# Performance work log

Measured on AMD Instinct MI355X. Metric: run time of the kernel, lower is better.

## Reference

```python
import jax, jax.numpy as jnp
import numpy as np

G, NPG, H, F, L = 2000, 16, 128, 28, 6   # graphs, nodes/graph, hidden, feat_dim, num_convs
N = G * NPG                               # 32000 nodes


def _build_graph():
    rng = np.random.default_rng(0)
    # global edges: all ordered intra-molecule pairs (dense radius graph)
    ii, jj = np.nonzero(1 - np.eye(NPG, dtype=np.int64))          # 240 pairs
    goff = np.arange(G, dtype=np.int64)[:, None] * NPG
    sg = (goff + ii[None]).ravel()
    dg = (goff + jj[None]).ravel()
    # local bond edges: ring per molecule, both directions
    li = np.arange(NPG, dtype=np.int64); lj = (li + 1) % NPG
    li2 = np.concatenate([li, lj]); lj2 = np.concatenate([lj, li])  # 32 per graph
    sl = (goff + li2[None]).ravel()
    dl = (goff + lj2[None]).ravel()
    etr = rng.integers(1, 22, size=(G, 2 * NPG)).astype(np.int64)   # bond types r
    etp = rng.integers(1, 22, size=(G, 2 * NPG)).astype(np.int64)   # bond types p
    # global types: local bond type where a bond exists, else 0 (clamped -1 sentinel)
    gidx = np.arange(G)[:, None]
    Tr = np.zeros((G, NPG, NPG), np.int64); Tp = np.zeros_like(Tr)
    Tr[gidx, li2[None], lj2[None]] = etr
    Tp[gidx, li2[None], lj2[None]] = etp
    egr = Tr[gidx, ii[None], jj[None]].ravel()
    egp = Tp[gidx, ii[None], jj[None]].ravel()
    return (np.stack([sl, dl]), etr.ravel(), etp.ravel(),
            np.stack([sg, dg]), egr, egp)


def setup_inputs() -> dict:
    key = jax.random.key(0)
    ks = jax.random.split(key, 24)
    eil, etr, etp, eig, egr, egp = _build_graph()
    n = lambda k, shp, fan: jax.random.normal(k, shp, jnp.float32) / np.sqrt(fan)
    inp = {
        'atom_type': jax.random.randint(ks[0], (N,), 0, 100),
        'r_feat': jax.random.normal(ks[1], (N, F), jnp.float32),
        'p_feat': jax.random.normal(ks[2], (N, F), jnp.float32),
        'pos': jax.random.normal(ks[3], (N, 3), jnp.float32),
        'edge_index_local': jnp.asarray(eil),
        'edge_type_r': jnp.asarray(etr),
        'edge_type_p': jnp.asarray(etp),
        'edge_index_global': jnp.asarray(eig),
        'edge_type_global_r': jnp.asarray(egr),
        'edge_type_global_p': jnp.asarray(egp),
        'bond_emb': n(ks[4], (100, H), 1.0),
        'atom_emb': n(ks[5], (100, H // 2), 1.0),
        'atom_feat_W': n(ks[6], (F, H // 2), F),
        'Wl': n(ks[7], (L, 4 * H, H), 4 * H), 'bl': jnp.zeros((L, H), jnp.float32),
        'Wg': n(ks[8], (L, 2 * H + 1, H), 2 * H + 1), 'bg': jnp.zeros((L, H), jnp.float32),
        'Wn': n(ks[9], (L, 2 * H, H), 2 * H), 'bn': jnp.zeros((L, H), jnp.float32),
        'W0': n(ks[10], (2 * H, H), 2 * H), 'b0': jnp.zeros((H,), jnp.float32),
        'W1': n(ks[11], (H, H // 2), H), 'b1': jnp.zeros((H // 2,), jnp.float32),
        'W2': n(ks[12], (H // 2, 1), H // 2), 'b2': jnp.zeros((1,), jnp.float32),
    }
    return inp


def reference(atom_type, r_feat, p_feat, pos,
              edge_index_local, edge_type_r, edge_type_p,
              edge_index_global, edge_type_global_r, edge_type_global_p,
              bond_emb, atom_emb, atom_feat_W,
              Wl, bl, Wg, bg, Wn, bn, W0, b0, W1, b1, W2, b2):
    num_nodes = atom_type.shape[0]
    # embedding gathers
    e_r = bond_emb[edge_type_r]            # [El,H]
    e_p = bond_emb[edge_type_p]
    e_gr = bond_emb[edge_type_global_r]    # [Eg,H]
    e_gp = bond_emb[edge_type_global_p]
    fr = r_feat @ atom_feat_W              # [N,H/2]
    fp = p_feat @ atom_feat_W
    h = jnp.concatenate([atom_emb[atom_type] + fr, fp - fr], axis=-1)  # [N,H]
    sl, dl = edge_index_local[0], edge_index_local[1]
    sg, dg = edge_index_global[0], edge_index_global[1]
    d2 = jnp.sum((pos[sg] - pos[dg]) ** 2, axis=-1, keepdims=True)     # [Eg,1]
    # EGNN mixed-2D encoder: local (bond) + global (radius) message passing
    for l in range(Wl.shape[0]):
        m_loc = jax.nn.silu(jnp.concatenate([h[sl], h[dl], e_r, e_p], -1) @ Wl[l] + bl[l])
        m_glb = jax.nn.silu(jnp.concatenate([h[sg], h[dg], d2], -1) @ Wg[l] + bg[l])
        agg = (jax.ops.segment_sum(m_loc, dl, num_segments=num_nodes)
               + jax.ops.segment_sum(m_glb, dg, num_segments=num_nodes))
        h = h + jax.nn.silu(jnp.concatenate([h, agg], -1) @ Wn[l] + bn[l])
    # node/edge pair products + output MLP (grad_dist_mlp), sigma_edge = 1.0
    h_pair = jnp.concatenate([h[sg] * h[dg], e_gr * e_gp], axis=-1)    # [Eg,2H]
    x = jax.nn.relu(h_pair @ W0 + b0)
    x = jax.nn.relu(x @ W1 + b1)
    edge_inv = x @ W2 + b2                                             # [Eg,1]
    return edge_inv
```

## Files before the change

### kernel.cpp

```cpp
#include <hip/hip_runtime.h>


#define G_GRAPHS 2000
#define NPG 16
#define HID 128
#define FDIM 28
#define NLAYER 6
#define NNODES 32000
#define EL_PER_G 32
#define EG_PER_G 240
#define EL_TOT (G_GRAPHS*EL_PER_G)
#define EG_TOT (G_GRAPHS*EG_PER_G)
#define TMAX 32

#define MC(r_, c_) ((r_)*HID + ((c_) ^ (((r_) & 7) << 3)))

typedef __attribute__((ext_vector_type(8))) short bf16x8;
typedef __attribute__((ext_vector_type(4))) float f32x4;

__device__ __forceinline__ float silu_f(float x) {
    return x * __builtin_amdgcn_rcpf(1.0f + __expf(-x));
}
__device__ __forceinline__ int clampT(int t) {
    return t < 0 ? 0 : (t > TMAX-1 ? TMAX-1 : t);
}
__device__ __forceinline__ unsigned short bf16_rne(float x) {
    unsigned u = __float_as_uint(x);
    return (unsigned short)((u + 0x7FFFu + ((u >> 16) & 1u)) >> 16);
}
__device__ __forceinline__ void split2(float x, unsigned short &hi, unsigned short &lo) {
    hi = bf16_rne(x);
    float fh = __uint_as_float((unsigned)hi << 16);
    lo = bf16_rne(x - fh);
}

__device__ __forceinline__ unsigned cvtpk(float a, float b) {
    unsigned r;
    asm("v_cvt_pk_bf16_f32 %0, %1, %2" : "=v"(r) : "v"(a), "v"(b));
    return r;
}

__device__ __forceinline__ void split8(const float* vv, bf16x8& h8, bf16x8& l8) {
    union { unsigned u[4]; bf16x8 v; } H, L;
    #pragma unroll
    for (int i = 0; i < 4; i++) {
        unsigned hp = cvtpk(vv[2*i], vv[2*i+1]);
        float fh0 = __uint_as_float(hp << 16);
        float fh1 = __uint_as_float(hp & 0xffff0000u);
        H.u[i] = hp;
        L.u[i] = cvtpk(vv[2*i] - fh0, vv[2*i+1] - fh1);
    }
    h8 = H.v; l8 = L.v;
}

template<int NT>
__device__ __forceinline__ void mm_nt_f32(const float* __restrict__ abuf,
                                          const unsigned short* __restrict__ Bh,
                                          const unsigned short* __restrict__ Bl,
                                          int ctbase, int lane, f32x4* acc) {
    const int n = lane & 15, kq = lane >> 4;
    const int sw = (n & 7) << 3;
    const float* ap = abuf + n*HID;
    const unsigned short* bh = Bh + ((size_t)(ctbase*4)*64 + lane)*8;
    const unsigned short* bl = Bl + ((size_t)(ctbase*4)*64 + lane)*8;
    #pragma unroll 1
    for (int kt = 0; kt < 4; kt++) {
        int idx = (kt*32 + kq*8) ^ sw;
        float4 v0 = *(const float4*)(ap + idx);
        float4 v1 = *(const float4*)(ap + idx + 4);
        float vv[8] = {v0.x, v0.y, v0.z, v0.w, v1.x, v1.y, v1.z, v1.w};
        bf16x8 ah, al;
        split8(vv, ah, al);
        const unsigned short* ph = bh;
        const unsigned short* pl = bl;
        #pragma unroll
        for (int t = 0; t < NT; t++) {
            bf16x8 vh = *(const bf16x8*)ph;
            bf16x8 vl = *(const bf16x8*)pl;
            acc[t] = __builtin_amdgcn_mfma_f32_16x16x32_bf16(ah, vh, acc[t], 0, 0, 0);
            acc[t] = __builtin_amdgcn_mfma_f32_16x16x32_bf16(ah, vl, acc[t], 0, 0, 0);
            acc[t] = __builtin_amdgcn_mfma_f32_16x16x32_bf16(al, vh, acc[t], 0, 0, 0);
            ph += 2048;
            pl += 2048;
        }
        bh += 512;
        bl += 512;
    }
}

__device__ __forceinline__ f32x4 mm_ct_s16(const short* __restrict__ ahbuf,
                                           const short* __restrict__ albuf,
                                           const unsigned short* __restrict__ Bh,
                                           const unsigned short* __restrict__ Bl,
                                           int ct, int lane, f32x4 acc) {
    const int n = lane & 15, kq = lane >> 4;
    const unsigned short* bh = Bh + ((size_t)(ct*4)*64 + lane)*8;
    const unsigned short* bl = Bl + ((size_t)(ct*4)*64 + lane)*8;
    #pragma unroll 1
    for (int kt = 0; kt < 4; kt++) {
        int sidx = (n*HID + kt*32 + kq*8) ^ ((n & 7) << 3);
        bf16x8 ah = *(const bf16x8*)(ahbuf + sidx);
        bf16x8 al = *(const bf16x8*)(albuf + sidx);
        bf16x8 vh = *(const bf16x8*)bh;
        bf16x8 vl = *(const bf16x8*)bl;
        acc = __builtin_amdgcn_mfma_f32_16x16x32_bf16(ah, vh, acc, 0, 0, 0);
        acc = __builtin_amdgcn_mfma_f32_16x16x32_bf16(ah, vl, acc, 0, 0, 0);
        acc = __builtin_amdgcn_mfma_f32_16x16x32_bf16(al, vh, acc, 0, 0, 0);
        bh += 512;
        bl += 512;
    }
    return acc;
}

__global__ void __launch_bounds__(256) k_pack(
    const float* __restrict__ Wg, const float* __restrict__ Wl,
    const float* __restrict__ Wn, const float* __restrict__ W0,
    const float* __restrict__ W1,
    unsigned short* __restrict__ encPh, unsigned short* __restrict__ encPl,
    unsigned short* __restrict__ w0Ph, unsigned short* __restrict__ w0Pl,
    unsigned short* __restrict__ w1Ph, unsigned short* __restrict__ w1Pl)
{
    int b = blockIdx.x, t = threadIdx.x;
    const float* src; int ldN, elems; unsigned short *dh, *dl;
    if (b < 36) {
        int l = b / 6, m = b % 6;
        src = (m == 0) ? Wg + (size_t)l*257*HID
            : (m == 1) ? Wg + (size_t)l*257*HID + 128*HID
            : (m == 2) ? Wl + (size_t)l*512*HID
            : (m == 3) ? Wl + (size_t)l*512*HID + 128*HID
            : (m == 4) ? Wn + (size_t)l*256*HID
            :            Wn + (size_t)l*256*HID + 128*HID;
        ldN = HID; elems = 16384;
        dh = encPh + (size_t)b*16384; dl = encPl + (size_t)b*16384;
    } else if (b == 36) {
        src = W0; ldN = HID; elems = 16384; dh = w0Ph; dl = w0Pl;
    } else {
        src = W1; ldN = 64; elems = 8192; dh = w1Ph; dl = w1Pl;
    }
    for (int idx = t; idx < elems; idx += 256) {
        int j = idx & 7, lane = (idx >> 3) & 63, kt = (idx >> 9) & 3, ct = idx >> 11;
        int k = kt*32 + (lane >> 4)*8 + j;
        int n = ct*16 + (lane & 15);
        unsigned short hi, lo;
        split2(src[(size_t)k*ldN + n], hi, lo);
        dh[idx] = hi; dl[idx] = lo;
    }
}

__global__ void __launch_bounds__(HID) k_tab_bond(
    const float* __restrict__ bond_emb, const float* __restrict__ Wl,
    const float* __restrict__ bl, float* __restrict__ bondA, float* __restrict__ bondB)
{
    int l = blockIdx.x >> 5, t = blockIdx.x & 31, c = threadIdx.x;
    const float* WlL = Wl + (size_t)l*512*HID;
    float accA = bl[l*HID + c], accB = 0.f;
    #pragma unroll 4
    for (int k = 0; k < HID; k++) {
        float e = bond_emb[t*HID + k];
        accA = fmaf(e, WlL[(256+k)*HID + c], accA);
        accB = fmaf(e, WlL[(384+k)*HID + c], accB);
    }
    bondA[(l*TMAX + t)*HID + c] = accA;
    bondB[(l*TMAX + t)*HID + c] = accB;
}

__global__ void __launch_bounds__(HID) k_tab_pair(
    const float* __restrict__ bond_emb, const float* __restrict__ W0,
    const float* __restrict__ b0, float* __restrict__ pairT)
{
    int tr = blockIdx.x >> 5, tp = blockIdx.x & 31, c = threadIdx.x;
    float acc = b0[c];
    #pragma unroll 4
    for (int k = 0; k < HID; k++)
        acc = fmaf(bond_emb[tr*HID + k] * bond_emb[tp*HID + k], W0[(HID+k)*HID + c], acc);
    pairT[(size_t)blockIdx.x*HID + c] = acc;
}

__global__ void __launch_bounds__(256) k_init_h(
    const int* __restrict__ atom_type, const float* __restrict__ r_feat,
    const float* __restrict__ p_feat, const float* __restrict__ atom_emb,
    const float* __restrict__ afW, float* __restrict__ h)
{
    int n = blockIdx.x*4 + (threadIdx.x >> 6);
    int j = threadIdx.x & 63;
    int at = atom_type[n];
    float accr = 0.f, accp = 0.f;
    #pragma unroll
    for (int k = 0; k < FDIM; k++) {
        float w = afW[k*64 + j];
        accr = fmaf(r_feat[n*FDIM + k], w, accr);
        accp = fmaf(p_feat[n*FDIM + k], w, accp);
    }
    h[n*HID + j]      = atom_emb[at*64 + j] + accr;
    h[n*HID + 64 + j] = accp - accr;
}

__global__ void __launch_bounds__(256, 4) k_encoder(
    const float* __restrict__ pos,
    const int* __restrict__ eil, const int* __restrict__ etr, const int* __restrict__ etp,
    const int* __restrict__ eig,
    const float* __restrict__ Wg, const float* __restrict__ bg,
    const float* __restrict__ bn,
    const float* __restrict__ bondA, const float* __restrict__ bondB,
    const unsigned short* __restrict__ encPh, const unsigned short* __restrict__ encPl,
    float* __restrict__ h)
{
    __shared__ __align__(16) float h_f[NPG*HID];
    __shared__ __align__(16) float M0[NPG*HID], M1[NPG*HID];
    __shared__ __align__(16) float M2[NPG*HID];
    __shared__ float d2m[NPG][NPG];
    __shared__ unsigned msk[NPG];
    __shared__ float px[NPG], py[NPG], pz[NPG];
    __shared__ int llist[NPG][2];
    __shared__ int lcnt[NPG];
    __shared__ int lsrc_s[EL_PER_G], ltr_s[EL_PER_G], ltp_s[EL_PER_G];

    const int g = blockIdx.x;
    const int tid = threadIdx.x;
    const int lane = tid & 63;
    const int w    = tid >> 6;
    const int c    = tid & 127;
    const int dh2  = tid >> 7;

    for (int idx = tid; idx < NPG*HID; idx += 256) {
        int n = idx >> 7, cc = idx & 127;
        h_f[MC(n, cc)] = h[(size_t)g*NPG*HID + idx];
    }
    if (tid < NPG) {
        px[tid] = pos[(g*NPG + tid)*3 + 0];
        py[tid] = pos[(g*NPG + tid)*3 + 1];
        pz[tid] = pos[(g*NPG + tid)*3 + 2];
        lcnt[tid] = 0; msk[tid] = 0u;
    }
    __syncthreads();
    if (tid < EG_PER_G) {
        int e = g*EG_PER_G + tid;
        int s = eig[e] - g*NPG;
        int d = eig[EG_TOT + e] - g*NPG;
        float dx = px[s]-px[d], dy = py[s]-py[d], dz = pz[s]-pz[d];
        d2m[d][s] = dx*dx + dy*dy + dz*dz;
        atomicOr(&msk[d], 1u << s);
    }
    if (tid < EL_PER_G) {
        int e = g*EL_PER_G + tid;
        int s = eil[e] - g*NPG;
        int d = eil[EL_TOT + e] - g*NPG;
        lsrc_s[tid] = s;
        ltr_s[tid] = clampT(etr[e]);
        ltp_s[tid] = clampT(etp[e]);
        int slot = atomicAdd(&lcnt[d], 1);
        if (slot < 2) llist[d][slot] = tid;
    }
    __syncthreads();

    const f32x4 zero = {0.f, 0.f, 0.f, 0.f};

    for (int l = 0; l < NLAYER; l++) {
        const unsigned short* baseH = encPh + (size_t)(l*6)*16384;
        const unsigned short* baseL = encPl + (size_t)(l*6)*16384;

        {
            int mat = w >> 1, ctbase = (w & 1) * 4;
            f32x4 acc[4] = {zero, zero, zero, zero};
            mm_nt_f32<4>(h_f, baseH + (size_t)mat*16384, baseL + (size_t)mat*16384,
                         ctbase, lane, acc);
            float* dst = mat ? M1 : M0;
            #pragma unroll
            for (int i = 0; i < 4; i++) {
                int n = (ctbase+i)*16 + (lane & 15);
                float bias = mat ? bg[l*HID + n] : 0.f;
                #pragma unroll
                for (int r = 0; r < 4; r++) {
                    int m = (lane >> 4)*4 + r;
                    dst[MC(m, n)] = acc[i][r] + bias;
                }
            }
        }
        __syncthreads();

        {
            float wgd = Wg[(size_t)l*257*HID + 256*HID + c];
            #pragma unroll 1
            for (int dd = 0; dd < 8; dd++) {
                int d = dh2*8 + dd;
                float base = M1[MC(d, c)];
                unsigned m = msk[d];
                float acc = 0.f;
                #pragma unroll
                for (int s = 0; s < NPG; s++) {
                    if (m & (1u << s)) {
                        float x = M0[MC(s, c)] + fmaf(d2m[d][s], wgd, base);
                        acc += silu_f(x);
                    }
                }
                M2[MC(d, c)] = acc;
            }
        }
        __syncthreads();

        {
            int mat = w >> 1, ctbase = (w & 1) * 4;
            f32x4 acc[4] = {zero, zero, zero, zero};
            mm_nt_f32<4>(h_f, baseH + (size_t)(2+mat)*16384, baseL + (size_t)(2+mat)*16384,
                         ctbase, lane, acc);
            float* dst = mat ? M1 : M0;
            #pragma unroll
            for (int i = 0; i < 4; i++) {
                int n = (ctbase+i)*16 + (lane & 15);
                #pragma unroll
                for (int r = 0; r < 4; r++) {
                    int m = (lane >> 4)*4 + r;
                    dst[MC(m, n)] = acc[i][r];
                }
            }
        }
        __syncthreads();

        {
            const float* bA = bondA + (size_t)l*TMAX*HID;
            const float* bB = bondB + (size_t)l*TMAX*HID;
            #pragma unroll 1
            for (int dd = 0; dd < 8; dd++) {
                int d = dh2*8 + dd;
                float acc = M2[MC(d, c)];
                float blb = M1[MC(d, c)];
                int lc2 = lcnt[d] < 2 ? lcnt[d] : 2;
                for (int i2 = 0; i2 < lc2; i2++) {
                    int ke = llist[d][i2];
                    float x = M0[MC(lsrc_s[ke], c)] + blb
                            + bA[ltr_s[ke]*HID + c] + bB[ltp_s[ke]*HID + c];
                    acc += silu_f(x);
                }
                M2[MC(d, c)] = acc;
            }
        }
        __syncthreads();

        {
            f32x4 acc[2] = {zero, zero};
            mm_nt_f32<2>(h_f, baseH + (size_t)4*16384, baseL + (size_t)4*16384,
                         w*2, lane, acc);
            mm_nt_f32<2>(M2,  baseH + (size_t)5*16384, baseL + (size_t)5*16384,
                         w*2, lane, acc);
            __syncthreads();
            #pragma unroll
            for (int i = 0; i < 2; i++) {
                int n = (w*2+i)*16 + (lane & 15);
                float bnv = bn[l*HID + n];
                #pragma unroll
                for (int r = 0; r < 4; r++) {
                    int m = (lane >> 4)*4 + r;
                    h_f[MC(m, n)] += silu_f(acc[i][r] + bnv);
                }
            }
        }
        __syncthreads();
    }

    for (int idx = tid; idx < NPG*HID; idx += 256) {
        int n = idx >> 7, cc = idx & 127;
        h[(size_t)g*NPG*HID + idx] = h_f[MC(n, cc)];
    }
}

__global__ void __launch_bounds__(256) k_mlp(
    const float* __restrict__ h,
    const int* __restrict__ eig, const int* __restrict__ egr, const int* __restrict__ egp,
    const float* __restrict__ pairT,
    const unsigned short* __restrict__ w0Ph, const unsigned short* __restrict__ w0Pl,
    const unsigned short* __restrict__ w1Ph, const unsigned short* __restrict__ w1Pl,
    const float* __restrict__ b1, const float* __restrict__ W2,
    const float* __restrict__ b2, float* __restrict__ out)
{
    __shared__ __align__(16) float h_s[NPG*HID];
    __shared__ __align__(16) short p_hi[NPG*HID], p_lo[NPG*HID];
    __shared__ __align__(16) short x_hi[NPG*HID], x_lo[NPG*HID];
    __shared__ int sgl[EG_PER_G], dgl[EG_PER_G], pidx[EG_PER_G];
    __shared__ float ypart[64];

    const int g = blockIdx.x;
    const int tid = threadIdx.x;
    const int lane = tid & 63;
    const int w = tid >> 6;

    for (int idx = tid; idx < NPG*HID; idx += 256)
        h_s[idx] = h[(size_t)g*NPG*HID + idx];
    if (tid < EG_PER_G) {
        int e = g*EG_PER_G + tid;
        sgl[tid] = eig[e] - g*NPG;
        dgl[tid] = eig[EG_TOT + e] - g*NPG;
        pidx[tid] = clampT(egr[e])*TMAX + clampT(egp[e]);
    }
    __syncthreads();
    const float b2v = b2[0];

    for (int e0 = 0; e0 < EG_PER_G; e0 += 16) {
        {
            int m = tid >> 4, c0 = (tid & 15) * 8;
            int e = e0 + m;
            const float* ps = h_s + sgl[e]*HID + c0;
            const float* pd = h_s + dgl[e]*HID + c0;
            float4 s0 = *(const float4*)ps, s1 = *(const float4*)(ps + 4);
            float4 d0 = *(const float4*)pd, d1 = *(const float4*)(pd + 4);
            float vv[8] = {s0.x*d0.x, s0.y*d0.y, s0.z*d0.z, s0.w*d0.w,
                           s1.x*d1.x, s1.y*d1.y, s1.z*d1.z, s1.w*d1.w};
            bf16x8 H8, L8;
            split8(vv, H8, L8);
            int sidx = (m*HID + c0) ^ ((m & 7) << 3);
            *(bf16x8*)&p_hi[sidx] = H8;
            *(bf16x8*)&p_lo[sidx] = L8;
        }
        __syncthreads();

        {
            #pragma unroll
            for (int i = 0; i < 2; i++) {
                int ct = w*2 + i;
                f32x4 acc = {0.f, 0.f, 0.f, 0.f};
                acc = mm_ct_s16(p_hi, p_lo, w0Ph, w0Pl, ct, lane, acc);
                int n = ct*16 + (lane & 15);
                #pragma unroll
                for (int r = 0; r < 4; r++) {
                    int m = (lane >> 4)*4 + r;
                    float x0v = acc[r] + pairT[(size_t)pidx[e0 + m]*HID + n];
                    x0v = fmaxf(x0v, 0.f);
                    unsigned short hi, lo;
                    split2(x0v, hi, lo);
                    int sidx = (m*HID + n) ^ ((m & 7) << 3);
                    x_hi[sidx] = (short)hi;
                    x_lo[sidx] = (short)lo;
                }
            }
        }
        __syncthreads();

        {
            f32x4 acc = {0.f, 0.f, 0.f, 0.f};
            acc = mm_ct_s16(x_hi, x_lo, w1Ph, w1Pl, w, lane, acc);
            int n = w*16 + (lane & 15);
            float b1v = b1[n], w2v = W2[n];
            float y[4];
            #pragma unroll
            for (int r = 0; r < 4; r++)
                y[r] = fmaxf(acc[r] + b1v, 0.f) * w2v;
            #pragma unroll
            for (int off = 1; off < 16; off <<= 1) {
                #pragma unroll
                for (int r = 0; r < 4; r++)
                    y[r] += __shfl_xor(y[r], off, 64);
            }
            if ((lane & 15) == 0) {
                #pragma unroll
                for (int r = 0; r < 4; r++)
                    ypart[w*16 + (lane >> 4)*4 + r] = y[r];
            }
        }
        __syncthreads();
        if (tid < 16)
            out[(size_t)g*EG_PER_G + e0 + tid] =
                ypart[tid] + ypart[16 + tid] + ypart[32 + tid] + ypart[48 + tid] + b2v;
        __syncthreads();
    }
}

extern "C" void kernel_launch(void* const* d_in, const int* in_sizes, int n_in,
                              void* d_out, int out_size, void* d_ws, size_t ws_size,
                              hipStream_t stream) {
    const int*   atom_type = (const int*)  d_in[0];
    const float* r_feat    = (const float*)d_in[1];
    const float* p_feat    = (const float*)d_in[2];
    const float* pos       = (const float*)d_in[3];
    const int*   eil       = (const int*)  d_in[4];
    const int*   etr       = (const int*)  d_in[5];
    const int*   etp       = (const int*)  d_in[6];
    const int*   eig       = (const int*)  d_in[7];
    const int*   egr       = (const int*)  d_in[8];
    const int*   egp       = (const int*)  d_in[9];
    const float* bond_emb  = (const float*)d_in[10];
    const float* atom_emb  = (const float*)d_in[11];
    const float* afW       = (const float*)d_in[12];
    const float* Wl        = (const float*)d_in[13];
    const float* bl        = (const float*)d_in[14];
    const float* Wg        = (const float*)d_in[15];
    const float* bg        = (const float*)d_in[16];
    const float* Wn        = (const float*)d_in[17];
    const float* bn        = (const float*)d_in[18];
    const float* W0        = (const float*)d_in[19];
    const float* b0        = (const float*)d_in[20];
    const float* W1        = (const float*)d_in[21];
    const float* b1        = (const float*)d_in[22];
    const float* W2        = (const float*)d_in[23];
    const float* b2        = (const float*)d_in[24];

    float* h     = (float*)d_ws;
    float* bondA = h + (size_t)NNODES*HID;
    float* bondB = bondA + (size_t)NLAYER*TMAX*HID;
    float* pairT = bondB + (size_t)NLAYER*TMAX*HID;
    unsigned short* encPh = (unsigned short*)(pairT + (size_t)TMAX*TMAX*HID);
    unsigned short* encPl = encPh + (size_t)36*16384;
    unsigned short* w0Ph  = encPl + (size_t)36*16384;
    unsigned short* w0Pl  = w0Ph + 16384;
    unsigned short* w1Ph  = w0Pl + 16384;
    unsigned short* w1Pl  = w1Ph + 8192;
    float* out   = (float*)d_out;

    k_pack    <<<dim3(38),          dim3(256), 0, stream>>>(Wg, Wl, Wn, W0, W1,
                                                            encPh, encPl, w0Ph, w0Pl, w1Ph, w1Pl);
    k_tab_bond<<<dim3(NLAYER*TMAX), dim3(HID), 0, stream>>>(bond_emb, Wl, bl, bondA, bondB);
    k_tab_pair<<<dim3(TMAX*TMAX),   dim3(HID), 0, stream>>>(bond_emb, W0, b0, pairT);
    k_init_h  <<<dim3(NNODES/4),    dim3(256), 0, stream>>>(atom_type, r_feat, p_feat, atom_emb, afW, h);
    k_encoder <<<dim3(G_GRAPHS),    dim3(256), 0, stream>>>(pos, eil, etr, etp, eig,
                                                            Wg, bg, bn, bondA, bondB,
                                                            encPh, encPl, h);
    k_mlp     <<<dim3(G_GRAPHS),    dim3(256), 0, stream>>>(h, eig, egr, egp, pairT,
                                                            w0Ph, w0Pl, w1Ph, w1Pl,
                                                            b1, W2, b2, out);
}
```

Baseline: 532.1 us.

## Give each wave its own 16-edge tile in the MLP kernel to drop barriers

The edge MLP kernel now hands each of the four waves a separate 16-edge tile with its own shared-memory scratch, instead of splitting every tile's columns across all waves. Each wave builds its pair products, runs all 8 first-layer column tiles and all 4 second-layer tiles itself, then reduces and writes outputs directly. This removes the block-wide __syncthreads and the cross-wave ypart reduction inside the edge loop. The cost is a serial chain of MFMA work per wave, 15 tiles spread unevenly over 4 waves (4/4/4/3), and more LDS per block, which may lower occupancy.

```diff
diff --git a/kernel.cpp b/kernel.cpp
--- a/kernel.cpp
+++ b/kernel.cpp
@@ -373,10 +373,9 @@
     const float* __restrict__ b2, float* __restrict__ out)
 {
     __shared__ __align__(16) float h_s[NPG*HID];
-    __shared__ __align__(16) short p_hi[NPG*HID], p_lo[NPG*HID];
-    __shared__ __align__(16) short x_hi[NPG*HID], x_lo[NPG*HID];
+    __shared__ __align__(16) short pw_hi[4][NPG*HID];
+    __shared__ __align__(16) short pw_lo[4][NPG*HID];
     __shared__ int sgl[EG_PER_G], dgl[EG_PER_G], pidx[EG_PER_G];
-    __shared__ float ypart[64];
 
     const int g = blockIdx.x;
     const int tid = threadIdx.x;
@@ -392,11 +391,21 @@
         pidx[tid] = clampT(egr[e])*TMAX + clampT(egp[e]);
     }
     __syncthreads();
+
     const float b2v = b2[0];
-
-    for (int e0 = 0; e0 < EG_PER_G; e0 += 16) {
-        {
-            int m = tid >> 4, c0 = (tid & 15) * 8;
+    short* ph = pw_hi[w];
+    short* pl = pw_lo[w];
+    const f32x4 zero = {0.f, 0.f, 0.f, 0.f};
+    const int nl = lane & 15;
+
+    for (int b = w; b < 15; b += 4) {
+        const int e0 = b * 16;
+
+        #pragma unroll
+        for (int i = 0; i < 4; i++) {
+            int q = i*64 + lane;
+            int m = q >> 4;
+            int c0 = (q & 15) * 8;
             int e = e0 + m;
             const float* ps = h_s + sgl[e]*HID + c0;
             const float* pd = h_s + dgl[e]*HID + c0;
@@ -407,59 +416,54 @@
             bf16x8 H8, L8;
             split8(vv, H8, L8);
             int sidx = (m*HID + c0) ^ ((m & 7) << 3);
-            *(bf16x8*)&p_hi[sidx] = H8;
-            *(bf16x8*)&p_lo[sidx] = L8;
-        }
-        __syncthreads();
-
-        {
-            #pragma unroll
-            for (int i = 0; i < 2; i++) {
-                int ct = w*2 + i;
-                f32x4 acc = {0.f, 0.f, 0.f, 0.f};
-                acc = mm_ct_s16(p_hi, p_lo, w0Ph, w0Pl, ct, lane, acc);
-                int n = ct*16 + (lane & 15);
-                #pragma unroll
-                for (int r = 0; r < 4; r++) {
-                    int m = (lane >> 4)*4 + r;
-                    float x0v = acc[r] + pairT[(size_t)pidx[e0 + m]*HID + n];
-                    x0v = fmaxf(x0v, 0.f);
-                    unsigned short hi, lo;
-                    split2(x0v, hi, lo);
-                    int sidx = (m*HID + n) ^ ((m & 7) << 3);
-                    x_hi[sidx] = (short)hi;
-                    x_lo[sidx] = (short)lo;
-                }
+            *(bf16x8*)&ph[sidx] = H8;
+            *(bf16x8*)&pl[sidx] = L8;
+        }
+
+        f32x4 a0[8];
+        #pragma unroll 1
+        for (int ct = 0; ct < 8; ct++)
+            a0[ct] = mm_ct_s16(ph, pl, w0Ph, w0Pl, ct, lane, zero);
+        #pragma unroll
+        for (int ct = 0; ct < 8; ct++) {
+            int ncol = ct*16 + nl;
+            #pragma unroll
+            for (int r = 0; r < 4; r++) {
+                int m = (lane >> 4)*4 + r;
+                float x0v = a0[ct][r] + pairT[(size_t)pidx[e0 + m]*HID + ncol];
+                x0v = fmaxf(x0v, 0.f);
+                unsigned short hi, lo;
+                split2(x0v, hi, lo);
+                int sidx = (m*HID + ncol) ^ ((m & 7) << 3);
+                ph[sidx] = (short)hi;
+                pl[sidx] = (short)lo;
             }
         }
-        __syncthreads();
-
-        {
-            f32x4 acc = {0.f, 0.f, 0.f, 0.f};
-            acc = mm_ct_s16(x_hi, x_lo, w1Ph, w1Pl, w, lane, acc);
-            int n = w*16 + (lane & 15);
-            float b1v = b1[n], w2v = W2[n];
-            float y[4];
+
+        f32x4 a1[4];
+        #pragma unroll 1
+        for (int ct = 0; ct < 4; ct++)
+            a1[ct] = mm_ct_s16(ph, pl, w1Ph, w1Pl, ct, lane, zero);
+        float part[4] = {0.f, 0.f, 0.f, 0.f};
+        #pragma unroll
+        for (int ct = 0; ct < 4; ct++) {
+            float b1v = b1[ct*16 + nl];
+            float w2v = W2[ct*16 + nl];
             #pragma unroll
             for (int r = 0; r < 4; r++)
-                y[r] = fmaxf(acc[r] + b1v, 0.f) * w2v;
-            #pragma unroll
-            for (int off = 1; off < 16; off <<= 1) {
-                #pragma unroll
-                for (int r = 0; r < 4; r++)
-                    y[r] += __shfl_xor(y[r], off, 64);
-            }
-            if ((lane & 15) == 0) {
-                #pragma unroll
-                for (int r = 0; r < 4; r++)
-                    ypart[w*16 + (lane >> 4)*4 + r] = y[r];
-            }
-        }
-        __syncthreads();
-        if (tid < 16)
-            out[(size_t)g*EG_PER_G + e0 + tid] =
-                ypart[tid] + ypart[16 + tid] + ypart[32 + tid] + ypart[48 + tid] + b2v;
-        __syncthreads();
+                part[r] += fmaxf(a1[ct][r] + b1v, 0.f) * w2v;
+        }
+        #pragma unroll
+        for (int off = 1; off < 16; off <<= 1) {
+            #pragma unroll
+            for (int r = 0; r < 4; r++)
+                part[r] += __shfl_xor(part[r], off, 64);
+        }
+        if (nl == 0) {
+            #pragma unroll
+            for (int r = 0; r < 4; r++)
+                out[(size_t)g*EG_PER_G + e0 + (lane >> 4)*4 + r] = part[r] + b2v;
+        }
     }
 }
 
```

Result: slower. 582.8 us (+9.5%).
